# Performance work log

Measured on AMD Instinct MI355X. Metric: run time of the kernel, lower is better.

## Reference

```python
import jax, jax.numpy as jnp
import numpy as np

B, C, H, W = 8, 64, 64, 64
A = C // 8  # attention_dim = 8


def setup_inputs() -> dict:
    key = jax.random.key(0)
    ks = jax.random.split(key, 6)
    x = jax.random.normal(ks[0], (B, C, H, W), dtype=jnp.float32)
    # 1x1 conv weights as [out, in] matrices (kernel_size=1)
    Wq = jax.random.normal(ks[1], (A, C), dtype=jnp.float32) * 0.05
    bq = jnp.zeros((A,), dtype=jnp.float32)
    Wk = jax.random.normal(ks[2], (A, C), dtype=jnp.float32) * 0.05
    bk = jnp.zeros((A,), dtype=jnp.float32)
    Wv = jax.random.normal(ks[3], (C, C), dtype=jnp.float32) * 0.05
    bv = jnp.zeros((C,), dtype=jnp.float32)
    gamma = jnp.array(0.01, dtype=jnp.float32)  # nn.Parameter(ones(1)*0.01)
    ln_w = jnp.ones((C,), dtype=jnp.float32)
    ln_b = jnp.zeros((C,), dtype=jnp.float32)
    return {"x": x, "Wq": Wq, "bq": bq, "Wk": Wk, "bk": bk,
            "Wv": Wv, "bv": bv, "gamma": gamma, "ln_w": ln_w, "ln_b": ln_b}


def reference(x, Wq, bq, Wk, bk, Wv, bv, gamma, ln_w, ln_b):
    b, c, h, w = x.shape
    n = h * w
    xf = x.reshape(b, c, n)  # [B, C, N]
    # 1x1 convs == per-pixel channel GEMMs
    q = jnp.einsum('ac,bcn->ban', Wq, xf) + bq[None, :, None]  # [B, A, N]
    k = jnp.einsum('ac,bcn->ban', Wk, xf) + bk[None, :, None]  # [B, A, N]
    v = jnp.einsum('oc,bcn->bon', Wv, xf) + bv[None, :, None]  # [B, C, N]
    # energy[b,n,m] = <Q[:, n], K[:, m]>  (NO 1/sqrt(d) scaling, as in source)
    energy = jnp.einsum('ban,bam->bnm', q, k)  # [B, N, N]
    attention = jax.nn.softmax(energy, axis=-1)
    # bmm(V, attention^T): out[b,c,n] = sum_m attention[b,n,m] * V[b,c,m]
    attn_out = jnp.einsum('bnm,bcm->bcn', attention, v).reshape(b, c, h, w)
    feature_delta = gamma * attn_out
    pre_norm = feature_delta + x
    # LayerNorm over channel dim (channels-last in source)
    y = jnp.transpose(pre_norm, (0, 2, 3, 1))  # [B, H, W, C]
    mu = jnp.mean(y, axis=-1, keepdims=True)
    var = jnp.var(y, axis=-1, keepdims=True)
    yn = (y - mu) * jax.lax.rsqrt(var + 1e-5) * ln_w + ln_b
    out = jnp.transpose(yn, (0, 3, 1, 2))  # [B, C, H, W]
    return (out, attention, feature_delta, attn_out)
```

## Files before the change

kernel.cpp:

```cpp
#include <hip/hip_runtime.h>

#define NPIX 4096
#define CCH  64
#define LOG2E 1.44269504088896f

typedef __attribute__((ext_vector_type(8))) short bf16x8;
typedef __attribute__((ext_vector_type(4))) float f32x4;

static __device__ __forceinline__ unsigned short f2bf(float f) {
    union { float f; unsigned u; } v; v.f = f;
    return (unsigned short)((v.u + 0x7FFFu + ((v.u >> 16) & 1u)) >> 16);
}
static __device__ __forceinline__ float bf2f_lo(unsigned u) {
    union { unsigned u; float f; } v; v.u = u << 16; return v.f;
}
static __device__ __forceinline__ float bf2f_hi(unsigned u) {
    union { unsigned u; float f; } v; v.u = u & 0xFFFF0000u; return v.f;
}


__global__ __launch_bounds__(256) void qkv_kernel(
    const float* __restrict__ x,
    const float* __restrict__ Wq, const float* __restrict__ bq,
    const float* __restrict__ Wk, const float* __restrict__ bk,
    const float* __restrict__ Wv, const float* __restrict__ bv,
    unsigned short* __restrict__ ws)
{
    __shared__ float xs[64][64];
    const int t  = threadIdx.x;
    const int b  = blockIdx.x >> 6;
    const int n0 = (blockIdx.x & 63) << 6;
    const float* xb = x + ((size_t)b * CCH) * NPIX;

    #pragma unroll
    for (int ii = 0; ii < 16; ++ii) {
        int idx = t + (ii << 8);
        int c = idx >> 6, nl = idx & 63;
        xs[c][nl] = xb[(size_t)c * NPIX + n0 + nl];
    }
    __syncthreads();

    const int nl = t & 63;
    const int og = t >> 6;
    unsigned short* qf = ws;
    unsigned short* kf = ws + 262144;
    unsigned short* vf = ws + 524288;
    const int n = n0 + nl;

    float xr[64];
    #pragma unroll
    for (int c = 0; c < 64; ++c) xr[c] = xs[c][nl];

    for (int oo = 0; oo < 20; ++oo) {
        const int o = og * 20 + oo;
        const float* Wrow;
        float bias;
        if (o < 8)       { Wrow = Wq + o * CCH;        bias = bq[o]; }
        else if (o < 16) { Wrow = Wk + (o - 8) * CCH;  bias = bk[o - 8]; }
        else             { Wrow = Wv + (o - 16) * CCH; bias = bv[o - 16]; }
        float acc = bias;
        #pragma unroll
        for (int c = 0; c < CCH; ++c) acc += Wrow[c] * xr[c];
        if (o < 8)       qf[((size_t)b * NPIX + n) * 8 + o] = f2bf(acc * LOG2E);
        else if (o < 16) kf[((size_t)b * NPIX + n) * 8 + (o - 8)] = f2bf(acc);
        else {
            const int c  = o - 16;
            const int kc = n >> 5, r5 = n & 31;
            const int lane = ((r5 >> 3) << 4) | (c & 15);
            const size_t idx = ((((size_t)b * 128 + kc) * 4 + (c >> 4)) * 64 + lane) * 8 + (r5 & 7);
            vf[idx] = f2bf(acc);
        }
    }
}

__global__ __launch_bounds__(256) void attn_kernel(
    const float* __restrict__ x, const unsigned short* __restrict__ ws,
    const float* __restrict__ gamma_p,
    const float* __restrict__ ln_w, const float* __restrict__ ln_b,
    float* __restrict__ out, float* __restrict__ attn,
    float* __restrict__ fd_out, float* __restrict__ ao_out)
{
    __shared__ __align__(16) char psb0[16384];
    __shared__ __align__(16) char psb1[16384];

    const int bid = blockIdx.x;
    const int wg  = ((bid & 7) << 7) | (bid >> 3);
    const int b   = wg >> 7;
    const int n0  = (wg & 127) << 5;

    const unsigned short* qf = ws;
    const unsigned short* kf = ws + 262144;
    const unsigned short* vf = ws + 524288;

    const int t   = threadIdx.x;
    const int l   = t & 63;
    const int w   = t >> 6;
    const int g   = l >> 4;
    const int c16 = l & 15;

    const unsigned short* qfb = qf + ((size_t)b * NPIX + n0) * 8;
    const unsigned short* kfb = kf + (size_t)b * NPIX * 8;
    const unsigned short* vwave = vf + (size_t)b * 128 * 2048 + w * 512;

    const f32x4 zf = {0.f, 0.f, 0.f, 0.f};

    bf16x8 QB0 = {}, QB1 = {};
    if (l < 16) {
        QB0 = *(const bf16x8*)(qfb + l * 8);
        QB1 = *(const bf16x8*)(qfb + (16 + l) * 8);
    }

    float s0 = 0.f, s1 = 0.f;
    #pragma unroll 4
    for (int mt = 0; mt < 64; ++mt) {
        const int mbase = (w << 10) + (mt << 4);
        bf16x8 Kf = {};
        if (l < 16) Kf = *(const bf16x8*)(kfb + (size_t)(mbase + l) * 8);
        f32x4 e0 = __builtin_amdgcn_mfma_f32_16x16x32_bf16(Kf, QB0, zf, 0, 0, 0);
        f32x4 e1 = __builtin_amdgcn_mfma_f32_16x16x32_bf16(Kf, QB1, zf, 0, 0, 0);
        #pragma unroll
        for (int r = 0; r < 4; ++r) {
            s0 += __builtin_amdgcn_exp2f(e0[r]);
            s1 += __builtin_amdgcn_exp2f(e1[r]);
        }
    }
    s0 += __shfl_xor(s0, 16); s0 += __shfl_xor(s0, 32);
    s1 += __shfl_xor(s1, 16); s1 += __shfl_xor(s1, 32);
    float lr0, lr1;
    {
        float* sred = (float*)psb0;
        if (l < 16) {
            sred[(w << 5) + l]      = s0;
            sred[(w << 5) + 16 + l] = s1;
        }
        __syncthreads();
        const float st0 = sred[c16]      + sred[32 + c16] + sred[64 + c16] + sred[96 + c16];
        const float st1 = sred[16 + c16] + sred[48 + c16] + sred[80 + c16] + sred[112 + c16];
        lr0 = -__builtin_amdgcn_logf(st0);
        lr1 = -__builtin_amdgcn_logf(st1);
        __syncthreads();
    }

    const int swx  = (c16 & 7) << 4;
    const int srow = (w << 3) + (l >> 3);
    const int ssw  = (srow & 7) << 4;
    const int srm  = (l & 7) << 3;
    float* arow = attn + ((size_t)b * NPIX + n0 + srow) * NPIX + ((l & 7) << 2);

    f32x4 acc0 = zf, acc1 = zf;

#define PHASE_A(MC, BUF) do {                                                     \
    _Pragma("unroll")                                                             \
    for (int j = 0; j < 4; ++j) {                                                 \
        const int mg = ((MC) << 8) + (w << 6) + (j << 4);                         \
        bf16x8 Kf = {};                                                           \
        if (l < 16) Kf = *(const bf16x8*)(kfb + (size_t)(mg + l) * 8);            \
        f32x4 e0 = __builtin_amdgcn_mfma_f32_16x16x32_bf16(Kf, QB0, zf, 0, 0, 0); \
        f32x4 e1 = __builtin_amdgcn_mfma_f32_16x16x32_bf16(Kf, QB1, zf, 0, 0, 0); \
        uint2 pk0, pk1;                                                           \
        pk0.x = (unsigned)f2bf(__builtin_amdgcn_exp2f(e0[0] + lr0))               \
              | ((unsigned)f2bf(__builtin_amdgcn_exp2f(e0[1] + lr0)) << 16);      \
        pk0.y = (unsigned)f2bf(__builtin_amdgcn_exp2f(e0[2] + lr0))               \
              | ((unsigned)f2bf(__builtin_amdgcn_exp2f(e0[3] + lr0)) << 16);      \
        pk1.x = (unsigned)f2bf(__builtin_amdgcn_exp2f(e1[0] + lr1))               \
              | ((unsigned)f2bf(__builtin_amdgcn_exp2f(e1[1] + lr1)) << 16);      \
        pk1.y = (unsigned)f2bf(__builtin_amdgcn_exp2f(e1[2] + lr1))               \
              | ((unsigned)f2bf(__builtin_amdgcn_exp2f(e1[3] + lr1)) << 16);      \
        const int wo = ((w << 7) + (j << 5) + (g << 3)) ^ swx;                    \
        *(uint2*)((BUF) + c16 * 512 + wo)        = pk0;                           \
        *(uint2*)((BUF) + (16 + c16) * 512 + wo) = pk1;                           \
    }                                                                             \
} while (0)

#define PHASE_B(MC, BUF) do {                                                     \
    const unsigned short* vbase = vwave + ((size_t)(MC) << 14);                   \
    __builtin_amdgcn_s_setprio(1);                                                \
    _Pragma("unroll")                                                             \
    for (int kc8 = 0; kc8 < 8; ++kc8) {                                           \
        const int aoff = ((kc8 << 6) | (g << 4)) ^ swx;                           \
        const bf16x8 Bf = *(const bf16x8*)(vbase + (size_t)kc8 * 2048 + l * 8);   \
        const bf16x8 A0 = *(const bf16x8*)((BUF) + c16 * 512 + aoff);             \
        const bf16x8 A1 = *(const bf16x8*)((BUF) + c16 * 512 + 8192 + aoff);      \
        acc0 = __builtin_amdgcn_mfma_f32_16x16x32_bf16(A0, Bf, acc0, 0, 0, 0);    \
        acc1 = __builtin_amdgcn_mfma_f32_16x16x32_bf16(A1, Bf, acc1, 0, 0, 0);    \
    }                                                                             \
    __builtin_amdgcn_s_setprio(0);                                                \
} while (0)

#define PHASE_S(MC, BUF) do {                                                     \
    _Pragma("unroll")                                                             \
    for (int i = 0; i < 8; ++i) {                                                 \
        const int ro = (srm + (i << 6)) ^ ssw;                                    \
        const uint2 rv = *(const uint2*)((BUF) + srow * 512 + ro);                \
        f32x4 fv;                                                                 \
        fv[0] = bf2f_lo(rv.x); fv[1] = bf2f_hi(rv.x);                             \
        fv[2] = bf2f_lo(rv.y); fv[3] = bf2f_hi(rv.y);                             \
        __builtin_nontemporal_store(fv, (f32x4*)(arow + ((MC) << 8) + (i << 5))); \
    }                                                                             \
} while (0)

    PHASE_A(0, psb0);
    __syncthreads();
    #pragma unroll 2
    for (int mc = 0; mc < 16; ++mc) {
        char* cur = (mc & 1) ? psb1 : psb0;
        char* nxt = (mc & 1) ? psb0 : psb1;
        PHASE_S(mc, cur);
        if (mc < 15) PHASE_A(mc + 1, nxt);
        PHASE_B(mc, cur);
        __syncthreads();
    }
#undef PHASE_A
#undef PHASE_B
#undef PHASE_S

    float* O_lds = (float*)psb0;
    float* muv   = (float*)(psb0 + 8448);
    float* rsg   = (float*)(psb0 + 8576);
    {
        const int ch = (w << 4) + c16;
        const int r0 = g << 2;
        #pragma unroll
        for (int r = 0; r < 4; ++r) {
            O_lds[ch * 33 + r0 + r]      = acc0[r];
            O_lds[ch * 33 + 16 + r0 + r] = acc1[r];
        }
    }
    __syncthreads();

    const float gma = gamma_p[0];
    const float* xb = x + (size_t)b * CCH * NPIX + n0;
    {
        const int r = t >> 3, l8 = t & 7;
        float sum = 0.f, sum2 = 0.f;
        #pragma unroll
        for (int cc = 0; cc < 8; ++cc) {
            const int c = l8 + (cc << 3);
            const float pre = xb[(size_t)c * NPIX + r] + gma * O_lds[c * 33 + r];
            sum += pre; sum2 += pre * pre;
        }
        #pragma unroll
        for (int off = 1; off < 8; off <<= 1) {
            sum  += __shfl_xor(sum, off);
            sum2 += __shfl_xor(sum2, off);
        }
        if (l8 == 0) {
            const float m_ = sum * (1.f / 64.f);
            const float v_ = sum2 * (1.f / 64.f) - m_ * m_;
            muv[r] = m_;
            rsg[r] = rsqrtf(v_ + 1e-5f);
        }
    }
    __syncthreads();

    #pragma unroll
    for (int ii = 0; ii < 8; ++ii) {
        const int idx = t + (ii << 8);
        const int c = idx >> 5, nl = idx & 31;
        const float o   = O_lds[c * 33 + nl];
        const float fdv = gma * o;
        const float pre = xb[(size_t)c * NPIX + nl] + fdv;
        const float y   = (pre - muv[nl]) * rsg[nl] * ln_w[c] + ln_b[c];
        const size_t off = (size_t)b * CCH * NPIX + (size_t)c * NPIX + n0 + nl;
        ao_out[off] = o;
        fd_out[off] = fdv;
        out[off]    = y;
    }
}

extern "C" void kernel_launch(void* const* d_in, const int* in_sizes, int n_in,
                              void* d_out, int out_size, void* d_ws, size_t ws_size,
                              hipStream_t stream) {
    const float* x     = (const float*)d_in[0];
    const float* Wq    = (const float*)d_in[1];
    const float* bq    = (const float*)d_in[2];
    const float* Wk    = (const float*)d_in[3];
    const float* bk    = (const float*)d_in[4];
    const float* Wv    = (const float*)d_in[5];
    const float* bv    = (const float*)d_in[6];
    const float* gamma = (const float*)d_in[7];
    const float* lnw   = (const float*)d_in[8];
    const float* lnb   = (const float*)d_in[9];

    float* out  = (float*)d_out;
    float* attn = out + 2097152;
    float* fd   = out + 136314880;
    float* ao   = out + 138412032;
    unsigned short* ws = (unsigned short*)d_ws;

    qkv_kernel<<<512, 256, 0, stream>>>(x, Wq, bq, Wk, bk, Wv, bv, ws);
    attn_kernel<<<1024, 256, 0, stream>>>(x, ws, gamma, lnw, lnb, out, attn, fd, ao);
}
```

Measured before the change: 171.3 us.

## Split attention key range across waves with private LDS and final reduction

```diff
diff --git a/kernel.cpp b/kernel.cpp
--- a/kernel.cpp
+++ b/kernel.cpp
@@ -80,8 +80,7 @@
     float* __restrict__ out, float* __restrict__ attn,
     float* __restrict__ fd_out, float* __restrict__ ao_out)
 {
-    __shared__ __align__(16) char psb0[16384];
-    __shared__ __align__(16) char psb1[16384];
+    __shared__ __align__(16) char smem[40960];
 
     const int bid = blockIdx.x;
     const int wg  = ((bid & 7) << 7) | (bid >> 3);
@@ -100,7 +99,7 @@
 
     const unsigned short* qfb = qf + ((size_t)b * NPIX + n0) * 8;
     const unsigned short* kfb = kf + (size_t)b * NPIX * 8;
-    const unsigned short* vwave = vf + (size_t)b * 128 * 2048 + w * 512;
+    const unsigned short* vfb = vf + (size_t)b * 128 * 2048;
 
     const f32x4 zf = {0.f, 0.f, 0.f, 0.f};
 
@@ -128,7 +127,7 @@
     s1 += __shfl_xor(s1, 16); s1 += __shfl_xor(s1, 32);
     float lr0, lr1;
     {
-        float* sred = (float*)psb0;
+        float* sred = (float*)smem;
         if (l < 16) {
             sred[(w << 5) + l]      = s0;
             sred[(w << 5) + 16 + l] = s1;
@@ -141,93 +140,85 @@
         __syncthreads();
     }
 
-    const int swx  = (c16 & 7) << 4;
-    const int srow = (w << 3) + (l >> 3);
-    const int ssw  = (srow & 7) << 4;
-    const int srm  = (l & 7) << 3;
-    float* arow = attn + ((size_t)b * NPIX + n0 + srow) * NPIX + ((l & 7) << 2);
-
-    f32x4 acc0 = zf, acc1 = zf;
-
-#define PHASE_A(MC, BUF) do {                                                     \
-    _Pragma("unroll")                                                             \
-    for (int j = 0; j < 4; ++j) {                                                 \
-        const int mg = ((MC) << 8) + (w << 6) + (j << 4);                         \
-        bf16x8 Kf = {};                                                           \
-        if (l < 16) Kf = *(const bf16x8*)(kfb + (size_t)(mg + l) * 8);            \
-        f32x4 e0 = __builtin_amdgcn_mfma_f32_16x16x32_bf16(Kf, QB0, zf, 0, 0, 0); \
-        f32x4 e1 = __builtin_amdgcn_mfma_f32_16x16x32_bf16(Kf, QB1, zf, 0, 0, 0); \
-        uint2 pk0, pk1;                                                           \
-        pk0.x = (unsigned)f2bf(__builtin_amdgcn_exp2f(e0[0] + lr0))               \
-              | ((unsigned)f2bf(__builtin_amdgcn_exp2f(e0[1] + lr0)) << 16);      \
-        pk0.y = (unsigned)f2bf(__builtin_amdgcn_exp2f(e0[2] + lr0))               \
-              | ((unsigned)f2bf(__builtin_amdgcn_exp2f(e0[3] + lr0)) << 16);      \
-        pk1.x = (unsigned)f2bf(__builtin_amdgcn_exp2f(e1[0] + lr1))               \
-              | ((unsigned)f2bf(__builtin_amdgcn_exp2f(e1[1] + lr1)) << 16);      \
-        pk1.y = (unsigned)f2bf(__builtin_amdgcn_exp2f(e1[2] + lr1))               \
-              | ((unsigned)f2bf(__builtin_amdgcn_exp2f(e1[3] + lr1)) << 16);      \
-        const int wo = ((w << 7) + (j << 5) + (g << 3)) ^ swx;                    \
-        *(uint2*)((BUF) + c16 * 512 + wo)        = pk0;                           \
-        *(uint2*)((BUF) + (16 + c16) * 512 + wo) = pk1;                           \
-    }                                                                             \
-} while (0)
-
-#define PHASE_B(MC, BUF) do {                                                     \
-    const unsigned short* vbase = vwave + ((size_t)(MC) << 14);                   \
-    __builtin_amdgcn_s_setprio(1);                                                \
-    _Pragma("unroll")                                                             \
-    for (int kc8 = 0; kc8 < 8; ++kc8) {                                           \
-        const int aoff = ((kc8 << 6) | (g << 4)) ^ swx;                           \
-        const bf16x8 Bf = *(const bf16x8*)(vbase + (size_t)kc8 * 2048 + l * 8);   \
-        const bf16x8 A0 = *(const bf16x8*)((BUF) + c16 * 512 + aoff);             \
-        const bf16x8 A1 = *(const bf16x8*)((BUF) + c16 * 512 + 8192 + aoff);      \
-        acc0 = __builtin_amdgcn_mfma_f32_16x16x32_bf16(A0, Bf, acc0, 0, 0, 0);    \
-        acc1 = __builtin_amdgcn_mfma_f32_16x16x32_bf16(A1, Bf, acc1, 0, 0, 0);    \
-    }                                                                             \
-    __builtin_amdgcn_s_setprio(0);                                                \
-} while (0)
-
-#define PHASE_S(MC, BUF) do {                                                     \
-    _Pragma("unroll")                                                             \
-    for (int i = 0; i < 8; ++i) {                                                 \
-        const int ro = (srm + (i << 6)) ^ ssw;                                    \
-        const uint2 rv = *(const uint2*)((BUF) + srow * 512 + ro);                \
-        f32x4 fv;                                                                 \
-        fv[0] = bf2f_lo(rv.x); fv[1] = bf2f_hi(rv.x);                             \
-        fv[2] = bf2f_lo(rv.y); fv[3] = bf2f_hi(rv.y);                             \
-        __builtin_nontemporal_store(fv, (f32x4*)(arow + ((MC) << 8) + (i << 5))); \
-    }                                                                             \
-} while (0)
-
-    PHASE_A(0, psb0);
-    __syncthreads();
+    char* myps = smem + w * 10240;
+    float* arow_s = attn + ((size_t)b * NPIX + n0) * NPIX + (w << 10) + (c16 << 2);
+
+    f32x4 acc[4][2];
+    #pragma unroll
+    for (int ct = 0; ct < 4; ++ct) { acc[ct][0] = zf; acc[ct][1] = zf; }
+
     #pragma unroll 2
     for (int mc = 0; mc < 16; ++mc) {
-        char* cur = (mc & 1) ? psb1 : psb0;
-        char* nxt = (mc & 1) ? psb0 : psb1;
-        PHASE_S(mc, cur);
-        if (mc < 15) PHASE_A(mc + 1, nxt);
-        PHASE_B(mc, cur);
-        __syncthreads();
-    }
-#undef PHASE_A
-#undef PHASE_B
-#undef PHASE_S
-
-    float* O_lds = (float*)psb0;
-    float* muv   = (float*)(psb0 + 8448);
-    float* rsg   = (float*)(psb0 + 8576);
-    {
-        const int ch = (w << 4) + c16;
-        const int r0 = g << 2;
-        #pragma unroll
-        for (int r = 0; r < 4; ++r) {
-            O_lds[ch * 33 + r0 + r]      = acc0[r];
-            O_lds[ch * 33 + 16 + r0 + r] = acc1[r];
-        }
-    }
-    __syncthreads();
-
+        char* slc = myps + (mc & 1) * 5120;
+        #pragma unroll
+        for (int j = 0; j < 4; ++j) {
+            const int mg = (w << 10) + (mc << 6) + (j << 4);
+            bf16x8 Kf = {};
+            if (l < 16) Kf = *(const bf16x8*)(kfb + (size_t)(mg + l) * 8);
+            f32x4 e0 = __builtin_amdgcn_mfma_f32_16x16x32_bf16(Kf, QB0, zf, 0, 0, 0);
+            f32x4 e1 = __builtin_amdgcn_mfma_f32_16x16x32_bf16(Kf, QB1, zf, 0, 0, 0);
+            uint2 pk0, pk1;
+            pk0.x = (unsigned)f2bf(__builtin_amdgcn_exp2f(e0[0] + lr0))
+                  | ((unsigned)f2bf(__builtin_amdgcn_exp2f(e0[1] + lr0)) << 16);
+            pk0.y = (unsigned)f2bf(__builtin_amdgcn_exp2f(e0[2] + lr0))
+                  | ((unsigned)f2bf(__builtin_amdgcn_exp2f(e0[3] + lr0)) << 16);
+            pk1.x = (unsigned)f2bf(__builtin_amdgcn_exp2f(e1[0] + lr1))
+                  | ((unsigned)f2bf(__builtin_amdgcn_exp2f(e1[1] + lr1)) << 16);
+            pk1.y = (unsigned)f2bf(__builtin_amdgcn_exp2f(e1[2] + lr1))
+                  | ((unsigned)f2bf(__builtin_amdgcn_exp2f(e1[3] + lr1)) << 16);
+            const int wo = c16 * 160 + (j << 5) + (g << 3);
+            *(uint2*)(slc + wo)        = pk0;
+            *(uint2*)(slc + 2560 + wo) = pk1;
+        }
+        __builtin_amdgcn_s_setprio(1);
+        #pragma unroll
+        for (int kc8 = 0; kc8 < 2; ++kc8) {
+            const bf16x8 A0 = *(const bf16x8*)(slc + c16 * 160 + (kc8 << 6) + (g << 4));
+            const bf16x8 A1 = *(const bf16x8*)(slc + c16 * 160 + 2560 + (kc8 << 6) + (g << 4));
+            const int kcg = (w << 5) + (mc << 1) + kc8;
+            #pragma unroll
+            for (int ct = 0; ct < 4; ++ct) {
+                const bf16x8 Bf = *(const bf16x8*)(vfb + ((size_t)(kcg * 4 + ct) * 64 + l) * 8);
+                acc[ct][0] = __builtin_amdgcn_mfma_f32_16x16x32_bf16(A0, Bf, acc[ct][0], 0, 0, 0);
+                acc[ct][1] = __builtin_amdgcn_mfma_f32_16x16x32_bf16(A1, Bf, acc[ct][1], 0, 0, 0);
+            }
+        }
+        __builtin_amdgcn_s_setprio(0);
+        #pragma unroll
+        for (int i = 0; i < 8; ++i) {
+            const int row = (i << 2) + g;
+            const uint2 rv = *(const uint2*)(slc + row * 160 + (c16 << 3));
+            f32x4 fv;
+            fv[0] = bf2f_lo(rv.x); fv[1] = bf2f_hi(rv.x);
+            fv[2] = bf2f_lo(rv.y); fv[3] = bf2f_hi(rv.y);
+            __builtin_nontemporal_store(fv,
+                (f32x4*)(arow_s + (size_t)row * NPIX + (mc << 6)));
+        }
+    }
+
+    __syncthreads();
+    float* ored = (float*)smem;
+    #pragma unroll
+    for (int ct = 0; ct < 4; ++ct)
+        #pragma unroll
+        for (int h = 0; h < 2; ++h)
+            #pragma unroll
+            for (int r = 0; r < 4; ++r)
+                ored[w * 2112 + (ct * 16 + c16) * 33 + (h << 4) + (g << 2) + r] = acc[ct][h][r];
+    __syncthreads();
+    #pragma unroll
+    for (int k = 0; k < 8; ++k) {
+        const int idx = t + (k << 8);
+        const int c = idx >> 5, r = idx & 31;
+        const float s = ored[c * 33 + r] + ored[2112 + c * 33 + r]
+                      + ored[4224 + c * 33 + r] + ored[6336 + c * 33 + r];
+        ored[c * 33 + r] = s;
+    }
+    __syncthreads();
+
+    float* O_lds = ored;
+    float* muv   = ored + 8448;
+    float* rsg   = ored + 8480;
     const float gma = gamma_p[0];
     const float* xb = x + (size_t)b * CCH * NPIX + n0;
     {
```

Result: slower. 209.4 us (+22.2%).
